# Optimization experiments

Hardware: AMD Instinct MI355X
Metric: run time of the kernel (lower is better)

The kernel has to match this reference:

```python
import jax, jax.numpy as jnp
import numpy as np

HIDDEN = 1024
INTER = 2048
NUM_EXPERTS = 8
TOP_K = 2
GROUP_SIZE = 128
TOKENS = 4096


def _dequant_int4(packed, scale, group_size):
    # packed: [E, N, K//2] ints in [0,256) holding two uint4 nibbles (low | high<<4)
    # scale:  [E, N, K//group_size] float32
    E, N, Kh = packed.shape
    K = 2 * Kh
    low = packed & 0xF
    high = (packed >> 4) & 0xF
    # interleave: even K positions = low nibble, odd = high nibble
    q = jnp.stack([low, high], axis=-1).reshape(E, N, K) - 8  # int4 values in [-8,7]
    q = q.astype(jnp.float32).reshape(E, N, K // group_size, group_size)
    w = q * scale[..., None]
    return w.reshape(E, N, K)


def setup_inputs() -> dict:
    key = jax.random.key(0)
    k1, k2, k3, k4, k5, k6 = jax.random.split(key, 6)
    x = jax.random.normal(k1, (TOKENS, HIDDEN), dtype=jnp.float32)
    router_w = jax.random.normal(k2, (NUM_EXPERTS, HIDDEN), dtype=jnp.float32) * 0.02
    w1 = jax.random.randint(k3, (NUM_EXPERTS, 2 * INTER, HIDDEN // 2), 0, 256, dtype=jnp.int32)
    w1_scale = jax.random.uniform(k4, (NUM_EXPERTS, 2 * INTER, HIDDEN // GROUP_SIZE), dtype=jnp.float32) * 0.05
    w2 = jax.random.randint(k5, (NUM_EXPERTS, HIDDEN, INTER // 2), 0, 256, dtype=jnp.int32)
    w2_scale = jax.random.uniform(k6, (NUM_EXPERTS, HIDDEN, INTER // GROUP_SIZE), dtype=jnp.float32) * 0.05
    return {"x": x, "router_w": router_w, "w1": w1, "w1_scale": w1_scale, "w2": w2, "w2_scale": w2_scale}


def reference(x, router_w, w1, w1_scale, w2, w2_scale):
    # Router: topk then softmax over the top-k logits
    scores = x @ router_w.T                                 # [T, E]
    top_w, top_i = jax.lax.top_k(scores, TOP_K)             # [T, K]
    top_w = jax.nn.softmax(top_w, axis=-1).astype(jnp.float32)

    # Dequantize int4 grouped weights once
    w1_deq = _dequant_int4(w1, w1_scale, GROUP_SIZE)        # [E, 2I, H]
    w2_deq = _dequant_int4(w2, w2_scale, GROUP_SIZE)        # [E, H, I]

    out = jnp.zeros_like(x)
    for e in range(NUM_EXPERTS):
        # per-token routing weight for expert e (0 if not routed)
        ge = jnp.sum(top_w * (top_i == e), axis=-1)         # [T]
        h = x @ w1_deq[e].T                                  # [T, 2I]
        gate, up = h[:, :INTER], h[:, INTER:]
        a = jax.nn.silu(gate) * up                           # SwiGLU
        y = a @ w2_deq[e].T                                  # [T, H]
        out = out + ge[:, None] * y
    return out
```

## Files before the change

### kernel.cpp

```cpp
#include <hip/hip_runtime.h>
#include <hip/hip_bf16.h>

#define HIDDEN 1024
#define INTER 2048
#define NE 8
#define GS 128
#define TOKENS 4096
#define MAXROWS 9216
#define MAXTILES 72

typedef __bf16 bf16x8 __attribute__((ext_vector_type(8)));
typedef float f32x4 __attribute__((ext_vector_type(4)));

#define OFF_TOPKI 0u
#define OFF_TOPKW 32768u
#define OFF_CTRL  65536u
#define OFF_TOK   66048u
#define OFF_SLOT  102912u
#define OFF_TILE  135680u
#define OFF_XB    139776u
#define OFF_A     8530432u
#define OFF_W1D   46279168u
#define OFF_W2D   113388032u
#define OFF_Y0    OFF_W1D
#define OFF_Y1    (OFF_W1D + 18874368u)

__device__ __forceinline__ unsigned short f2bf(float f) {
  union { float f; unsigned int u; } v; v.f = f;
  unsigned int r = (v.u + 0x7FFFu + ((v.u >> 16) & 1u)) >> 16;
  return (unsigned short)r;
}
__device__ __forceinline__ float bf2f(unsigned int u) {
  union { unsigned int u; float f; } v; v.u = u << 16;
  return v.f;
}
__device__ __forceinline__ unsigned int pack2(unsigned short lo, unsigned short hi) {
  return (unsigned int)lo | ((unsigned int)hi << 16);
}

typedef const __attribute__((address_space(1))) unsigned int GAS;
typedef __attribute__((address_space(3))) unsigned int LAS;
__device__ __forceinline__ void gload16(const unsigned short* g, unsigned short* l) {
  __builtin_amdgcn_global_load_lds((GAS*)g, (LAS*)l, 16, 0, 0);
}


__global__ __launch_bounds__(256) void k_prep(const float* __restrict__ x,
    const float* __restrict__ rw, int* __restrict__ topki, float* __restrict__ topkw,
    const int* __restrict__ w1, const float* __restrict__ w1s,
    unsigned short* __restrict__ w1d,
    const int* __restrict__ w2, const float* __restrict__ w2s,
    unsigned short* __restrict__ w2d, unsigned short* __restrict__ xb) {
  int bid = blockIdx.x, tid = threadIdx.x;
  if (bid == 29696) {
    uint2 z; z.x = 0u; z.y = 0u;
    *reinterpret_cast<uint2*>(xb + (size_t)TOKENS * HIDDEN + tid * 4) = z;
    return;
  }
  if (bid >= 25600) {
    size_t idx = (size_t)(bid - 25600) * 1024 + tid * 4;
    float4 v = *reinterpret_cast<const float4*>(x + idx);
    uint2 o;
    o.x = pack2(f2bf(v.x), f2bf(v.y));
    o.y = pack2(f2bf(v.z), f2bf(v.w));
    *reinterpret_cast<uint2*>(xb + idx) = o;
    return;
  }
  if (bid >= 17408) {
    int gid = (bid - 17408) * 256 + tid;
    int i4 = gid * 4;
    int r = i4 >> 10;
    int i = i4 & 1023;
    float s = w2s[r * 16 + (i >> 6)];
    int4 p = *reinterpret_cast<const int4*>(w2 + (size_t)i4);
    int pv[4] = { p.x, p.y, p.z, p.w };
    uint4 o; unsigned int ov[4];
#pragma unroll
    for (int j = 0; j < 4; j++) {
      float lo = (float)((pv[j] & 15) - 8) * s;
      float hi = (float)(((pv[j] >> 4) & 15) - 8) * s;
      ov[j] = pack2(f2bf(lo), f2bf(hi));
    }
    o.x = ov[0]; o.y = ov[1]; o.z = ov[2]; o.w = ov[3];
    *reinterpret_cast<uint4*>(w2d + ((size_t)r << 11) + 2 * i) = o;
    return;
  }
  if (bid >= 1024) {
    int gid = (bid - 1024) * 256 + tid;
    int i4 = gid * 4;
    int r = i4 >> 9;
    int i = i4 & 511;
    float s = w1s[r * 8 + (i >> 6)];
    int4 p = *reinterpret_cast<const int4*>(w1 + (size_t)i4);
    int pv[4] = { p.x, p.y, p.z, p.w };
    uint4 o; unsigned int ov[4];
#pragma unroll
    for (int j = 0; j < 4; j++) {
      float lo = (float)((pv[j] & 15) - 8) * s;
      float hi = (float)(((pv[j] >> 4) & 15) - 8) * s;
      ov[j] = pack2(f2bf(lo), f2bf(hi));
    }
    o.x = ov[0]; o.y = ov[1]; o.z = ov[2]; o.w = ov[3];
    *reinterpret_cast<uint4*>(w1d + ((size_t)r << 10) + 2 * i) = o;
    return;
  }
  int wave = tid >> 6, lane = tid & 63;
  int t = bid * 4 + wave;
  float acc[NE];
#pragma unroll
  for (int e = 0; e < NE; e++) acc[e] = 0.f;
  const float* xr = x + (size_t)t * HIDDEN;
  for (int i = lane; i < HIDDEN; i += 64) {
    float xv = xr[i];
#pragma unroll
    for (int e = 0; e < NE; e++) acc[e] += xv * rw[e * HIDDEN + i];
  }
#pragma unroll
  for (int e = 0; e < NE; e++) {
    float v = acc[e];
    for (int off = 32; off > 0; off >>= 1) v += __shfl_down(v, off, 64);
    acc[e] = v;
  }
  if (lane == 0) {
    int b0 = 0; float s0 = acc[0];
#pragma unroll
    for (int e = 1; e < NE; e++) if (acc[e] > s0) { s0 = acc[e]; b0 = e; }
    int b1 = -1; float s1 = -3.0e38f;
#pragma unroll
    for (int e = 0; e < NE; e++) if (e != b0 && acc[e] > s1) { s1 = acc[e]; b1 = e; }
    float w0 = 1.f / (1.f + __expf(s1 - s0));
    topki[t * 2] = b0; topki[t * 2 + 1] = b1;
    topkw[t * 2] = w0; topkw[t * 2 + 1] = 1.f - w0;
  }
}

__global__ __launch_bounds__(256) void k_route2(const int* __restrict__ topki,
    int* __restrict__ ctrl, int* __restrict__ tok, int* __restrict__ slots,
    int* __restrict__ tilemap) {
  __shared__ int h[NE], off[NE], cnt[NE];
  int tid = threadIdx.x;
  if (tid < NE) h[tid] = 0;
  __syncthreads();
  for (int i = tid; i < TOKENS * 2; i += 256) atomicAdd(&h[topki[i]], 1);
  __syncthreads();
  if (tid == 0) {
    int run = 0, t = 0;
    for (int e = 0; e < NE; e++) {
      int c = h[e];
      ctrl[e] = c; ctrl[16 + e] = run; off[e] = run;
      int pc = (c + 127) & ~127;
      for (int mt = 0; mt < (pc >> 7); mt++) tilemap[t++] = (e << 20) | (run + mt * 128);
      run += pc;
    }
    ctrl[24] = run; ctrl[25] = t;
  }
  __syncthreads();
#pragma unroll
  for (int e = 0; e < NE; e++) {
    int c = h[e], pc = (c + 127) & ~127;
    for (int i = c + tid; i < pc; i += 256) tok[off[e] + i] = -1;
  }
  if (tid < NE) cnt[tid] = off[tid];
  __syncthreads();
  for (int i = tid; i < TOKENS * 2; i += 256) {
    int e = topki[i];
    int p = atomicAdd(&cnt[e], 1);
    tok[p] = i >> 1;
    slots[i] = p;
  }
}

__global__ __launch_bounds__(256) void k_gemm1(
    const unsigned short* __restrict__ xb, const unsigned short* __restrict__ w1d,
    const int* __restrict__ ctrl, const int* __restrict__ tilemap,
    const int* __restrict__ tok, unsigned short* __restrict__ a_out) {
  __shared__ unsigned short sA[128 * 32];
  __shared__ unsigned short sBg[64 * 32];
  __shared__ unsigned short sBu[64 * 32];
  int bid = blockIdx.x, tid = threadIdx.x;
  int nt = bid & 31, tile = bid >> 5;
  if (tile >= ctrl[25]) return;
  int tm = tilemap[tile];
  int e = tm >> 20, row0 = tm & 0xFFFFF;
  int n0 = nt * 64;
  int wave = tid >> 6, lane = tid & 63;
  int ln = lane & 15, quad = lane >> 4;
  int wr = (wave & 1) * 64, wc = (wave >> 1) * 32;

  int srow = tid >> 2, scblk = tid & 3;
  int scol = (scblk ^ ((srow >> 1) & 3)) * 8;
  int t0 = tok[row0 + srow];
  int t1 = tok[row0 + 64 + srow];
  const unsigned short* gA0 = xb + (size_t)(t0 < 0 ? TOKENS : t0) * HIDDEN + scol;
  const unsigned short* gA1 = xb + (size_t)(t1 < 0 ? TOKENS : t1) * HIDDEN + scol;
  const unsigned short* gBg = w1d + ((size_t)e * 4096 + n0 + srow) * HIDDEN + scol;
  const unsigned short* gBu = gBg + (size_t)INTER * HIDDEN;
  unsigned short* lA0 = sA + tid * 8;
  unsigned short* lA1 = sA + 64 * 32 + tid * 8;
  unsigned short* lBg = sBg + tid * 8;
  unsigned short* lBu = sBu + tid * 8;

  f32x4 aG[4][2] = {}, aU[4][2] = {};
  for (int k0 = 0; k0 < HIDDEN; k0 += 32) {
    __syncthreads();
    gload16(gA0 + k0, lA0);
    gload16(gA1 + k0, lA1);
    gload16(gBg + k0, lBg);
    gload16(gBu + k0, lBu);
    __syncthreads();
    bf16x8 af[4], bg[2], bu[2];
#pragma unroll
    for (int m = 0; m < 4; m++) {
      int ar = wr + m * 16 + ln;
      af[m] = *reinterpret_cast<const bf16x8*>(&sA[ar * 32 + (quad ^ ((ar >> 1) & 3)) * 8]);
    }
#pragma unroll
    for (int n = 0; n < 2; n++) {
      int br = wc + n * 16 + ln;
      int bo = br * 32 + (quad ^ ((br >> 1) & 3)) * 8;
      bg[n] = *reinterpret_cast<const bf16x8*>(&sBg[bo]);
      bu[n] = *reinterpret_cast<const bf16x8*>(&sBu[bo]);
    }
#pragma unroll
    for (int m = 0; m < 4; m++)
#pragma unroll
      for (int n = 0; n < 2; n++) {
        aG[m][n] = __builtin_amdgcn_mfma_f32_16x16x32_bf16(af[m], bg[n], aG[m][n], 0, 0, 0);
        aU[m][n] = __builtin_amdgcn_mfma_f32_16x16x32_bf16(af[m], bu[n], aU[m][n], 0, 0, 0);
      }
  }
#pragma unroll
  for (int m = 0; m < 4; m++)
#pragma unroll
    for (int n = 0; n < 2; n++) {
      int col = n0 + wc + n * 16 + ln;
#pragma unroll
      for (int r = 0; r < 4; r++) {
        float g = aG[m][n][r], u = aU[m][n][r];
        float act = (g / (1.f + __expf(-g))) * u;
        int row = row0 + wr + m * 16 + quad * 4 + r;
        a_out[(size_t)row * INTER + col] = f2bf(act);
      }
    }
}

__global__ __launch_bounds__(256) void k_gemm2(
    const unsigned short* __restrict__ a_in, const unsigned short* __restrict__ w2d,
    const int* __restrict__ ctrl, const int* __restrict__ tilemap,
    unsigned short* __restrict__ y) {
  __shared__ unsigned short sA[128 * 32];
  __shared__ unsigned short sB[128 * 32];
  int bid = blockIdx.x, tid = threadIdx.x;
  int kp = bid & 1, nt = (bid >> 1) & 7, tile = bid >> 4;
  if (tile >= ctrl[25]) return;
  int tm = tilemap[tile];
  int e = tm >> 20, row0 = tm & 0xFFFFF;
  int n0 = nt * 128;
  int wave = tid >> 6, lane = tid & 63;
  int ln = lane & 15, quad = lane >> 4;
  int wr = (wave & 1) * 64, wc = (wave >> 1) * 64;

  int srow = tid >> 2, scblk = tid & 3;
  int scol = (scblk ^ ((srow >> 1) & 3)) * 8;
  int kbase = kp * (INTER / 2);
  const unsigned short* gA0 = a_in + (size_t)(row0 + srow) * INTER + kbase + scol;
  const unsigned short* gA1 = gA0 + (size_t)64 * INTER;
  const unsigned short* gB0 = w2d + ((size_t)e * 1024 + n0 + srow) * INTER + kbase + scol;
  const unsigned short* gB1 = gB0 + (size_t)64 * INTER;
  unsigned short* lA0 = sA + tid * 8;
  unsigned short* lA1 = sA + 64 * 32 + tid * 8;
  unsigned short* lB0 = sB + tid * 8;
  unsigned short* lB1 = sB + 64 * 32 + tid * 8;

  f32x4 acc[4][4] = {};
  for (int k0 = 0; k0 < INTER / 2; k0 += 32) {
    __syncthreads();
    gload16(gA0 + k0, lA0);
    gload16(gA1 + k0, lA1);
    gload16(gB0 + k0, lB0);
    gload16(gB1 + k0, lB1);
    __syncthreads();
    bf16x8 af[4], bf_[4];
#pragma unroll
    for (int m = 0; m < 4; m++) {
      int ar = wr + m * 16 + ln;
      af[m] = *reinterpret_cast<const bf16x8*>(&sA[ar * 32 + (quad ^ ((ar >> 1) & 3)) * 8]);
    }
#pragma unroll
    for (int n = 0; n < 4; n++) {
      int br = wc + n * 16 + ln;
      bf_[n] = *reinterpret_cast<const bf16x8*>(&sB[br * 32 + (quad ^ ((br >> 1) & 3)) * 8]);
    }
#pragma unroll
    for (int m = 0; m < 4; m++)
#pragma unroll
      for (int n = 0; n < 4; n++)
        acc[m][n] = __builtin_amdgcn_mfma_f32_16x16x32_bf16(af[m], bf_[n], acc[m][n], 0, 0, 0);
  }
  unsigned short* yk = y + (size_t)kp * MAXROWS * HIDDEN;
#pragma unroll
  for (int m = 0; m < 4; m++)
#pragma unroll
    for (int n = 0; n < 4; n++) {
      int col = n0 + wc + n * 16 + ln;
#pragma unroll
      for (int r = 0; r < 4; r++) {
        int row = row0 + wr + m * 16 + quad * 4 + r;
        yk[(size_t)row * HIDDEN + col] = f2bf(acc[m][n][r]);
      }
    }
}

__global__ __launch_bounds__(256) void k_combine(const unsigned short* __restrict__ y,
    const int* __restrict__ slots, const float* __restrict__ topkw,
    float* __restrict__ out) {
  int t = blockIdx.x;
  int c = threadIdx.x * 4;
  int s0 = slots[t * 2], s1 = slots[t * 2 + 1];
  float g0 = topkw[t * 2], g1 = topkw[t * 2 + 1];
  const unsigned short* y1 = y + (size_t)MAXROWS * HIDDEN;
  uint2 a0 = *reinterpret_cast<const uint2*>(y  + (size_t)s0 * HIDDEN + c);
  uint2 a1 = *reinterpret_cast<const uint2*>(y1 + (size_t)s0 * HIDDEN + c);
  uint2 b0 = *reinterpret_cast<const uint2*>(y  + (size_t)s1 * HIDDEN + c);
  uint2 b1 = *reinterpret_cast<const uint2*>(y1 + (size_t)s1 * HIDDEN + c);
  float4 o;
  o.x = g0 * (bf2f(a0.x & 0xffffu) + bf2f(a1.x & 0xffffu))
      + g1 * (bf2f(b0.x & 0xffffu) + bf2f(b1.x & 0xffffu));
  o.y = g0 * (bf2f(a0.x >> 16) + bf2f(a1.x >> 16))
      + g1 * (bf2f(b0.x >> 16) + bf2f(b1.x >> 16));
  o.z = g0 * (bf2f(a0.y & 0xffffu) + bf2f(a1.y & 0xffffu))
      + g1 * (bf2f(b0.y & 0xffffu) + bf2f(b1.y & 0xffffu));
  o.w = g0 * (bf2f(a0.y >> 16) + bf2f(a1.y >> 16))
      + g1 * (bf2f(b0.y >> 16) + bf2f(b1.y >> 16));
  *reinterpret_cast<float4*>(out + (size_t)t * HIDDEN + c) = o;
}

extern "C" void kernel_launch(void* const* d_in, const int* in_sizes, int n_in,
                              void* d_out, int out_size, void* d_ws, size_t ws_size,
                              hipStream_t stream) {
  const float* x   = (const float*)d_in[0];
  const float* rw  = (const float*)d_in[1];
  const int*   w1  = (const int*)d_in[2];
  const float* w1s = (const float*)d_in[3];
  const int*   w2  = (const int*)d_in[4];
  const float* w2s = (const float*)d_in[5];
  float* out = (float*)d_out;
  char* ws = (char*)d_ws;

  int*   topki = (int*)(ws + OFF_TOPKI);
  float* topkw = (float*)(ws + OFF_TOPKW);
  int*   ctrl  = (int*)(ws + OFF_CTRL);
  int*   tok   = (int*)(ws + OFF_TOK);
  int*   slots = (int*)(ws + OFF_SLOT);
  int*   tilemap = (int*)(ws + OFF_TILE);
  unsigned short* xb  = (unsigned short*)(ws + OFF_XB);
  unsigned short* a   = (unsigned short*)(ws + OFF_A);
  unsigned short* w1d = (unsigned short*)(ws + OFF_W1D);
  unsigned short* w2d = (unsigned short*)(ws + OFF_W2D);
  unsigned short* y   = (unsigned short*)(ws + OFF_Y0);

  k_prep<<<29697, 256, 0, stream>>>(x, rw, topki, topkw, w1, w1s, w1d, w2, w2s, w2d, xb);
  k_route2<<<1, 256, 0, stream>>>(topki, ctrl, tok, slots, tilemap);
  k_gemm1<<<32 * MAXTILES, 256, 0, stream>>>(xb, w1d, ctrl, tilemap, tok, a);
  k_gemm2<<<16 * MAXTILES, 256, 0, stream>>>(a, w2d, ctrl, tilemap, y);
  k_combine<<<TOKENS, 256, 0, stream>>>(y, slots, topkw, out);
}
```

Measured before the change: 320.2 us.

## Fuse combine into gemm2 via gated atomic scatter and fold x conversion into router

The separate combine kernel and the bf16 intermediate y buffers are removed. gemm2 now multiplies each row by its routing gate and atomically adds it into the fp32 output at the owning token, with the output zeroed by a memset beforehand. The x-to-bf16 conversion moves into the router loop, which already reads x, so the dedicated conversion blocks are dropped. This saves y write and read traffic and one launch, but adds float atomics (two split-K halves and two experts per output element), a memset, and nondeterministic summation order.

Measured after the change: 360.9 us. 12.7% more time.

```diff
diff --git a/kernel.cpp b/kernel.cpp
--- a/kernel.cpp
+++ b/kernel.cpp
@@ -16,23 +16,17 @@
 #define OFF_TOPKW 32768u
 #define OFF_CTRL  65536u
 #define OFF_TOK   66048u
-#define OFF_SLOT  102912u
-#define OFF_TILE  135680u
-#define OFF_XB    139776u
-#define OFF_A     8530432u
-#define OFF_W1D   46279168u
-#define OFF_W2D   113388032u
-#define OFF_Y0    OFF_W1D
-#define OFF_Y1    (OFF_W1D + 18874368u)
+#define OFF_GATE  102912u
+#define OFF_TILE  139776u
+#define OFF_XB    140288u
+#define OFF_A     8530944u
+#define OFF_W1D   46279680u
+#define OFF_W2D   113388544u
 
 __device__ __forceinline__ unsigned short f2bf(float f) {
   union { float f; unsigned int u; } v; v.f = f;
   unsigned int r = (v.u + 0x7FFFu + ((v.u >> 16) & 1u)) >> 16;
   return (unsigned short)r;
-}
-__device__ __forceinline__ float bf2f(unsigned int u) {
-  union { unsigned int u; float f; } v; v.u = u << 16;
-  return v.f;
 }
 __device__ __forceinline__ unsigned int pack2(unsigned short lo, unsigned short hi) {
   return (unsigned int)lo | ((unsigned int)hi << 16);
@@ -52,18 +46,9 @@
     const int* __restrict__ w2, const float* __restrict__ w2s,
     unsigned short* __restrict__ w2d, unsigned short* __restrict__ xb) {
   int bid = blockIdx.x, tid = threadIdx.x;
-  if (bid == 29696) {
+  if (bid == 25600) {
     uint2 z; z.x = 0u; z.y = 0u;
     *reinterpret_cast<uint2*>(xb + (size_t)TOKENS * HIDDEN + tid * 4) = z;
-    return;
-  }
-  if (bid >= 25600) {
-    size_t idx = (size_t)(bid - 25600) * 1024 + tid * 4;
-    float4 v = *reinterpret_cast<const float4*>(x + idx);
-    uint2 o;
-    o.x = pack2(f2bf(v.x), f2bf(v.y));
-    o.y = pack2(f2bf(v.z), f2bf(v.w));
-    *reinterpret_cast<uint2*>(xb + idx) = o;
     return;
   }
   if (bid >= 17408) {
@@ -110,8 +95,10 @@
 #pragma unroll
   for (int e = 0; e < NE; e++) acc[e] = 0.f;
   const float* xr = x + (size_t)t * HIDDEN;
+  unsigned short* xbr = xb + (size_t)t * HIDDEN;
   for (int i = lane; i < HIDDEN; i += 64) {
     float xv = xr[i];
+    xbr[i] = f2bf(xv);
 #pragma unroll
     for (int e = 0; e < NE; e++) acc[e] += xv * rw[e * HIDDEN + i];
   }
@@ -135,8 +122,8 @@
 }
 
 __global__ __launch_bounds__(256) void k_route2(const int* __restrict__ topki,
-    int* __restrict__ ctrl, int* __restrict__ tok, int* __restrict__ slots,
-    int* __restrict__ tilemap) {
+    const float* __restrict__ topkw, int* __restrict__ ctrl, int* __restrict__ tok,
+    float* __restrict__ gate, int* __restrict__ tilemap) {
   __shared__ int h[NE], off[NE], cnt[NE];
   int tid = threadIdx.x;
   if (tid < NE) h[tid] = 0;
@@ -166,7 +153,7 @@
     int e = topki[i];
     int p = atomicAdd(&cnt[e], 1);
     tok[p] = i >> 1;
-    slots[i] = p;
+    gate[p] = topkw[i];
   }
 }
 
@@ -247,15 +234,22 @@
 __global__ __launch_bounds__(256) void k_gemm2(
     const unsigned short* __restrict__ a_in, const unsigned short* __restrict__ w2d,
     const int* __restrict__ ctrl, const int* __restrict__ tilemap,
-    unsigned short* __restrict__ y) {
+    const int* __restrict__ tok, const float* __restrict__ gate,
+    float* __restrict__ out) {
   __shared__ unsigned short sA[128 * 32];
   __shared__ unsigned short sB[128 * 32];
+  __shared__ int stok[128];
+  __shared__ float sgate[128];
   int bid = blockIdx.x, tid = threadIdx.x;
   int kp = bid & 1, nt = (bid >> 1) & 7, tile = bid >> 4;
   if (tile >= ctrl[25]) return;
   int tm = tilemap[tile];
   int e = tm >> 20, row0 = tm & 0xFFFFF;
   int n0 = nt * 128;
+  if (tid < 128) {
+    stok[tid] = tok[row0 + tid];
+    sgate[tid] = gate[row0 + tid];
+  }
   int wave = tid >> 6, lane = tid & 63;
   int ln = lane & 15, quad = lane >> 4;
   int wr = (wave & 1) * 64, wc = (wave >> 1) * 64;
@@ -297,7 +291,6 @@
       for (int n = 0; n < 4; n++)
         acc[m][n] = __builtin_amdgcn_mfma_f32_16x16x32_bf16(af[m], bf_[n], acc[m][n], 0, 0, 0);
   }
-  unsigned short* yk = y + (size_t)kp * MAXROWS * HIDDEN;
 #pragma unroll
   for (int m = 0; m < 4; m++)
 #pragma unroll
@@ -305,34 +298,11 @@
       int col = n0 + wc + n * 16 + ln;
 #pragma unroll
       for (int r = 0; r < 4; r++) {
-        int row = row0 + wr + m * 16 + quad * 4 + r;
-        yk[(size_t)row * HIDDEN + col] = f2bf(acc[m][n][r]);
+        int rl = wr + m * 16 + quad * 4 + r;
+        int t = stok[rl];
+        if (t >= 0) atomicAdd(out + (size_t)t * HIDDEN + col, sgate[rl] * acc[m][n][r]);
       }
     }
-}
-
-__global__ __launch_bounds__(256) void k_combine(const unsigned short* __restrict__ y,
-    const int* __restrict__ slots, const float* __restrict__ topkw,
-    float* __restrict__ out) {
-  int t = blockIdx.x;
-  int c = threadIdx.x * 4;
-  int s0 = slots[t * 2], s1 = slots[t * 2 + 1];
-  float g0 = topkw[t * 2], g1 = topkw[t * 2 + 1];
-  const unsigned short* y1 = y + (size_t)MAXROWS * HIDDEN;
-  uint2 a0 = *reinterpret_cast<const uint2*>(y  + (size_t)s0 * HIDDEN + c);
-  uint2 a1 = *reinterpret_cast<const uint2*>(y1 + (size_t)s0 * HIDDEN + c);
-  uint2 b0 = *reinterpret_cast<const uint2*>(y  + (size_t)s1 * HIDDEN + c);
-  uint2 b1 = *reinterpret_cast<const uint2*>(y1 + (size_t)s1 * HIDDEN + c);
-  float4 o;
-  o.x = g0 * (bf2f(a0.x & 0xffffu) + bf2f(a1.x & 0xffffu))
-      + g1 * (bf2f(b0.x & 0xffffu) + bf2f(b1.x & 0xffffu));
-  o.y = g0 * (bf2f(a0.x >> 16) + bf2f(a1.x >> 16))
-      + g1 * (bf2f(b0.x >> 16) + bf2f(b1.x >> 16));
-  o.z = g0 * (bf2f(a0.y & 0xffffu) + bf2f(a1.y & 0xffffu))
-      + g1 * (bf2f(b0.y & 0xffffu) + bf2f(b1.y & 0xffffu));
-  o.w = g0 * (bf2f(a0.y >> 16) + bf2f(a1.y >> 16))
-      + g1 * (bf2f(b0.y >> 16) + bf2f(b1.y >> 16));
-  *reinterpret_cast<float4*>(out + (size_t)t * HIDDEN + c) = o;
 }
 
 extern "C" void kernel_launch(void* const* d_in, const int* in_sizes, int n_in,
@@ -351,17 +321,16 @@
   float* topkw = (float*)(ws + OFF_TOPKW);
   int*   ctrl  = (int*)(ws + OFF_CTRL);
   int*   tok   = (int*)(ws + OFF_TOK);
-  int*   slots = (int*)(ws + OFF_SLOT);
+  float* gate  = (float*)(ws + OFF_GATE);
   int*   tilemap = (int*)(ws + OFF_TILE);
   unsigned short* xb  = (unsigned short*)(ws + OFF_XB);
   unsigned short* a   = (unsigned short*)(ws + OFF_A);
   unsigned short* w1d = (unsigned short*)(ws + OFF_W1D);
   unsigned short* w2d = (unsigned short*)(ws + OFF_W2D);
-  unsigned short* y   = (unsigned short*)(ws + OFF_Y0);
-
-  k_prep<<<29697, 256, 0, stream>>>(x, rw, topki, topkw, w1, w1s, w1d, w2, w2s, w2d, xb);
-  k_route2<<<1, 256, 0, stream>>>(topki, ctrl, tok, slots, tilemap);
+
+  k_prep<<<25601, 256, 0, stream>>>(x, rw, topki, topkw, w1, w1s, w1d, w2, w2s, w2d, xb);
+  k_route2<<<1, 256, 0, stream>>>(topki, topkw, ctrl, tok, gate, tilemap);
+  hipMemsetAsync(out, 0, (size_t)out_size * sizeof(float), stream);
   k_gemm1<<<32 * MAXTILES, 256, 0, stream>>>(xb, w1d, ctrl, tilemap, tok, a);
-  k_gemm2<<<16 * MAXTILES, 256, 0, stream>>>(a, w2d, ctrl, tilemap, y);
-  k_combine<<<TOKENS, 256, 0, stream>>>(y, slots, topkw, out);
-}
+  k_gemm2<<<16 * MAXTILES, 256, 0, stream>>>(a, w2d, ctrl, tilemap, tok, gate, out);
+}
```
